# Kernel tuning notes

Hardware: AMD Instinct MI355X
Metric: run time of the kernel (lower is better)

## Reference

```python
import jax, jax.numpy as jnp
import numpy as np

NEG_INF = -1.0e9  # matches the -1000000000.0 additive mask in the source


def setup_inputs() -> dict:
    key = jax.random.key(0)
    kq, kk, kv = jax.random.split(key, 3)
    B, Lq, Lk, D = 16, 2048, 2048, 128
    q = jax.random.normal(kq, (B, Lq, D), dtype=jnp.float32)
    k = jax.random.normal(kk, (B, Lk, D), dtype=jnp.float32)
    v = jax.random.normal(kv, (B, Lk, D), dtype=jnp.float32)
    mask = jnp.ones((B, Lq, Lk), dtype=jnp.int32)  # 1 = attend, 0 = blocked
    return {"q": q, "k": k, "v": v, "mask": mask}


def reference(q, k, v, mask):
    # temper = sqrt(d_k)
    temper = jnp.sqrt(jnp.asarray(q.shape[-1], dtype=jnp.float32))
    # scores: [B, Lq, Lk] = batch_dot(q, k, axes=[2,2]) / temper
    scores = jnp.einsum("bqd,bkd->bqk", q, k) / temper
    # additive mask: -1e9 * (1 - mask)
    scores = scores + NEG_INF * (1.0 - mask.astype(jnp.float32))
    attn = jax.nn.softmax(scores, axis=-1)
    # dropout is identity at inference time
    out = jnp.einsum("bqk,bkd->bqd", attn, v)
    return (out, attn)
```

## Files before the change

kernel.cpp:

```cpp
#include <hip/hip_runtime.h>

typedef __bf16 bf16_t;
typedef __bf16 bf16x8 __attribute__((ext_vector_type(8)));
typedef __bf16 bf16x4 __attribute__((ext_vector_type(4)));
typedef float  f32x4  __attribute__((ext_vector_type(4)));
typedef int    i32x4  __attribute__((ext_vector_type(4)));

#define B_      16
#define L_      2048
#define D_      128
#define QTB     128
#define NEGINF  (-1.0e9f)
#define SCALE   0.08838834764831845f

#define MFMA_BF16 __builtin_amdgcn_mfma_f32_16x16x32_bf16

#define BARRIER() do { asm volatile("s_waitcnt lgkmcnt(0)" ::: "memory"); \
                       __builtin_amdgcn_s_barrier(); } while (0)

__global__ __launch_bounds__(256) void prep_kernel(
    const float* __restrict__ k, const float* __restrict__ v,
    bf16_t* __restrict__ kb, bf16_t* __restrict__ vt)
{
    __shared__ bf16_t tile[128 * 144];
    const int tid = threadIdx.x;
    const int bid = (int)blockIdx.x;

    if (bid < 256) {
        const int b  = bid >> 4;
        const int l0 = (bid & 15) * 128;
        #pragma unroll
        for (int it = 0; it < 16; ++it) {
            int idx = tid + it * 256;
            int row = idx >> 5;
            int dc4 = idx & 31;
            f32x4 x = __builtin_nontemporal_load(
                (const f32x4*)(v + ((size_t)b * L_ + l0 + row) * (size_t)D_ + dc4 * 4));
            #pragma unroll
            for (int i = 0; i < 4; ++i) tile[(dc4 * 4 + i) * 144 + row] = (bf16_t)x[i];
        }
        __syncthreads();
        #pragma unroll
        for (int it = 0; it < 8; ++it) {
            int idx = tid + it * 256;
            int d   = idx >> 4;
            int lc  = idx & 15;
            bf16x8 vec = *(const bf16x8*)&tile[d * 144 + lc * 8];
            *(bf16x8*)(vt + ((size_t)b * D_ + d) * (size_t)L_ + l0 + lc * 8) = vec;
        }
    } else {
        const int idx0 = (bid - 256) * 256 + tid;
        #pragma unroll
        for (int c = 0; c < 16; ++c) {
            int idx = idx0 + c * 65536;
            f32x4 x = __builtin_nontemporal_load((const f32x4*)(k + (size_t)idx * 4));
            bf16x4 o;
            #pragma unroll
            for (int i = 0; i < 4; ++i) o[i] = (bf16_t)x[i];
            *(bf16x4*)(kb + (size_t)idx * 4) = o;
        }
    }
}

template <bool WS>
__global__ __launch_bounds__(512, 1) void sdpa_kernel(
    const float* __restrict__ q, const float* __restrict__ k,
    const float* __restrict__ v, const int* __restrict__ mask,
    const bf16_t* __restrict__ kb, const bf16_t* __restrict__ vt,
    float* __restrict__ out, float* __restrict__ attn)
{
    __shared__ char     Kst[2][16384];
    __shared__ char     MV[2][32768];
    __shared__ unsigned mlds[8 * 1024];
    __shared__ bf16_t   plds[8][16][40];

    const int tid = threadIdx.x;
    const int w   = tid >> 6;
    const int l   = tid & 63;
    const int li  = l & 15;
    const int lg  = l >> 4;

    const int bid  = (int)blockIdx.x;
    const int bid2 = (bid & 7) * 32 + (bid >> 3);
    const int b    = bid2 >> 4;
    const int qt   = bid2 & 15;
    const int qbase = qt * QTB;

    const size_t bq = (size_t)b * L_;

    const float*  qp  = q  + (bq + qbase) * (size_t)D_;
    const bf16_t* kbp = kb + bq * (size_t)D_;
    const float*  kp  = k  + bq * (size_t)D_;
    const bf16_t* vtp = vt + (size_t)b * D_ * (size_t)L_;
    const float*  vp  = v  + bq * (size_t)D_;
    float* attnrow = attn + (bq + qbase + (size_t)(w * 16 + li)) * (size_t)L_;
    float* outp    = out  + (bq + qbase) * (size_t)D_;

    bf16x8 aq[4];
    #pragma unroll
    for (int ds = 0; ds < 4; ++ds) {
        const float* p = qp + (size_t)(w * 16 + li) * D_ + ds * 32 + lg * 8;
        f32x4 x0 = *(const f32x4*)p;
        f32x4 x1 = *(const f32x4*)(p + 4);
        bf16x8 a;
        #pragma unroll
        for (int u = 0; u < 4; ++u) {
            a[u]     = (bf16_t)(x0[u] * SCALE);
            a[4 + u] = (bf16_t)(x1[u] * SCALE);
        }
        aq[ds] = a;
    }

    const int ku_t  = (tid >> 6) & 1;
    const int ku_lg = (tid >> 4) & 3;
    const int ku_li = tid & 15;
    const int ku_ds = tid >> 7;
    const bf16_t* ksrcb = kbp + (size_t)(ku_t * 16 + ku_li) * D_ + ku_ds * 32 + ku_lg * 8;
    const float*  ksrcf = kp  + (size_t)(ku_t * 16 + ku_li) * D_ + ku_ds * 32 + ku_lg * 8;

    const int vu_d  = ((tid >> 6) << 4) | (tid & 15);
    const int vu_lg = (tid >> 4) & 3;
    const bf16_t* vsrcb = vtp + (size_t)vu_d * L_ + vu_lg * 8;

    const int mrow = tid >> 3, mslot = tid & 7;
    const int mdst0 = mrow * 128 + ((mslot * 16) ^ ((mrow & 7) << 4));
    const int mdst1 = (mrow + 64) * 128 + ((mslot * 16) ^ ((mrow & 7) << 4));
    const int*    msrc0 = mask + (size_t)(bq + qbase + mrow) * L_ + mslot * 4;
    const int*    msrc1 = mask + (size_t)(bq + qbase + mrow + 64) * L_ + mslot * 4;

    auto issueK = [&](int t, i32x4 (&ri)[2], f32x4 (&rf)[2][2]) {
        #pragma unroll
        for (int s = 0; s < 2; ++s) {
            if constexpr (WS) {
                ri[s] = *(const i32x4*)(ksrcb + (size_t)(t * 64 + s * 32) * D_);
            } else {
                rf[s][0] = *(const f32x4*)(ksrcf + (size_t)(t * 64 + s * 32) * D_);
                rf[s][1] = *(const f32x4*)(ksrcf + (size_t)(t * 64 + s * 32) * D_ + 4);
            }
        }
    };
    auto writeK = [&](int sl, const i32x4 (&ri)[2], const f32x4 (&rf)[2][2]) {
        #pragma unroll
        for (int s = 0; s < 2; ++s) {
            char* d = Kst[sl] + s * 8192 + tid * 16;
            if constexpr (WS) {
                *(i32x4*)d = ri[s];
            } else {
                bf16x8 o;
                #pragma unroll
                for (int u = 0; u < 4; ++u) { o[u] = (bf16_t)rf[s][0][u]; o[4+u] = (bf16_t)rf[s][1][u]; }
                *(bf16x8*)d = o;
            }
        }
    };
    auto issueM = [&](int t, i32x4 (&m0)[2], i32x4 (&m1)[2]) {
        #pragma unroll
        for (int s = 0; s < 2; ++s) {
            m0[s] = __builtin_nontemporal_load((const i32x4*)(msrc0 + t * 64 + s * 32));
            m1[s] = __builtin_nontemporal_load((const i32x4*)(msrc1 + t * 64 + s * 32));
        }
    };
    auto writeM = [&](int sl, const i32x4 (&m0)[2], const i32x4 (&m1)[2]) {
        #pragma unroll
        for (int s = 0; s < 2; ++s) {
            *(i32x4*)(MV[sl] + s * 16384 + mdst0) = m0[s];
            *(i32x4*)(MV[sl] + s * 16384 + mdst1) = m1[s];
        }
    };
    auto issueV = [&](int t, i32x4 (&ri)[2], float (&vf)[2][8]) {
        #pragma unroll
        for (int s = 0; s < 2; ++s) {
            if constexpr (WS) {
                ri[s] = *(const i32x4*)(vsrcb + t * 64 + s * 32);
            } else {
                #pragma unroll
                for (int u = 0; u < 8; ++u)
                    vf[s][u] = vp[(size_t)(t * 64 + s * 32 + vu_lg * 8 + u) * D_ + vu_d];
            }
        }
    };
    auto writeV = [&](int sl, const i32x4 (&ri)[2], const float (&vf)[2][8]) {
        #pragma unroll
        for (int s = 0; s < 2; ++s) {
            char* d = MV[sl] + s * 8192 + tid * 16;
            if constexpr (WS) {
                *(i32x4*)d = ri[s];
            } else {
                bf16x8 o;
                #pragma unroll
                for (int u = 0; u < 8; ++u) o[u] = (bf16_t)vf[s][u];
                *(bf16x8*)d = o;
            }
        }
    };

    const int xr = (li & 7) << 4;
    const int kbo = lg * 256 + li * 16;

    auto qkt = [&](const char* Ks, f32x4& a0, f32x4& a1) {
        f32x4 r0 = {0.f,0.f,0.f,0.f}, r1 = {0.f,0.f,0.f,0.f};
        #pragma unroll
        for (int ds = 0; ds < 4; ++ds) {
            bf16x8 k0 = *(const bf16x8*)(Ks + ds * 2048 + kbo);
            r0 = MFMA_BF16(k0, aq[ds], r0, 0, 0, 0);
        }
        #pragma unroll
        for (int ds = 0; ds < 4; ++ds) {
            bf16x8 k1 = *(const bf16x8*)(Ks + ds * 2048 + 1024 + kbo);
            r1 = MFMA_BF16(k1, aq[ds], r1, 0, 0, 0);
        }
        a0 = r0; a1 = r1;
    };

    float m_run = -3.4e38f, l_run = 0.f;
    {
        unsigned mword = 0;
        auto p1c = [&](int m, int sl, int s) {
            f32x4 a0, a1;
            qkt(Kst[sl] + s * 8192, a0, a1);
            const char* Ms = MV[sl] + s * 16384 + (w * 16 + li) * 128;
            i32x4 va  = *(const i32x4*)(Ms + ((lg * 16) ^ xr));
            i32x4 vb_ = *(const i32x4*)(Ms + ((64 + lg * 16) ^ xr));
            unsigned byte =
                (va[0]  != 0 ?   1u : 0u) | (va[1]  != 0 ?   2u : 0u) |
                (va[2]  != 0 ?   4u : 0u) | (va[3]  != 0 ?   8u : 0u) |
                (vb_[0] != 0 ?  16u : 0u) | (vb_[1] != 0 ?  32u : 0u) |
                (vb_[2] != 0 ?  64u : 0u) | (vb_[3] != 0 ? 128u : 0u);
            float s0[4], s1[4];
            #pragma unroll
            for (int r = 0; r < 4; ++r) {
                s0[r] = a0[r] + (((byte >> r)       & 1u) ? 0.f : NEGINF);
                s1[r] = a1[r] + (((byte >> (4 + r)) & 1u) ? 0.f : NEGINF);
            }
            float mx = fmaxf(fmaxf(fmaxf(s0[0], s0[1]), fmaxf(s0[2], s0[3])),
                             fmaxf(fmaxf(s1[0], s1[1]), fmaxf(s1[2], s1[3])));
            mx = fmaxf(mx, m_run);
            float acc = 0.f;
            #pragma unroll
            for (int r = 0; r < 4; ++r)
                acc += __expf(s0[r] - mx) + __expf(s1[r] - mx);
            l_run = l_run * __expf(m_run - mx) + acc;
            m_run = mx;
            mword |= byte << ((m & 3) * 8);
            if ((m & 3) == 3) { mlds[w * 1024 + (m >> 2) * 64 + l] = mword; mword = 0; }
        };

        i32x4 kA[2]{}, kB[2]{}, m0A[2]{}, m1A[2]{}, m0B[2]{}, m1B[2]{};
        f32x4 kfA[2][2], kfB[2][2];
        issueK(0, kA, kfA); issueM(0, m0A, m1A);
        issueK(1, kB, kfB); issueM(1, m0B, m1B);
        writeK(0, kA, kfA); writeM(0, m0A, m1A);
        BARRIER();
        #pragma unroll 1
        for (int t = 0; t < 32; t += 2) {
            if (t + 2 < 32) { issueK(t + 2, kA, kfA); issueM(t + 2, m0A, m1A); }
            p1c(2 * t,     0, 0);
            p1c(2 * t + 1, 0, 1);
            writeK(1, kB, kfB); writeM(1, m0B, m1B);
            BARRIER();
            if (t + 3 < 32) { issueK(t + 3, kB, kfB); issueM(t + 3, m0B, m1B); }
            p1c(2 * t + 2, 1, 0);
            p1c(2 * t + 3, 1, 1);
            if (t + 2 < 32) { writeK(0, kA, kfA); writeM(0, m0A, m1A); }
            BARRIER();
        }
    }

    #pragma unroll
    for (int off = 16; off < 64; off <<= 1) {
        float mo = __shfl_xor(m_run, off);
        float lo = __shfl_xor(l_run, off);
        float mn = fmaxf(m_run, mo);
        l_run = l_run * __expf(m_run - mn) + lo * __expf(mo - mn);
        m_run = mn;
    }
    const float inv_l = 1.f / l_run;

    f32x4 pv[8];
    #pragma unroll
    for (int dt = 0; dt < 8; ++dt) pv[dt] = {0.f, 0.f, 0.f, 0.f};

    {
        auto p2c = [&](int m, int sl, int s) {
            f32x4 a0, a1;
            qkt(Kst[sl] + s * 8192, a0, a1);
            const unsigned mw = mlds[w * 1024 + (m >> 2) * 64 + l];
            const unsigned byte = (mw >> ((m & 3) * 8)) & 0xffu;
            f32x4 o0, o1; bf16x4 pb0, pb1;
            #pragma unroll
            for (int r = 0; r < 4; ++r) {
                float sa = a0[r] + (((byte >> r)       & 1u) ? 0.f : NEGINF);
                float sb = a1[r] + (((byte >> (4 + r)) & 1u) ? 0.f : NEGINF);
                float p0 = __expf(sa - m_run);
                float p1 = __expf(sb - m_run);
                o0[r] = p0 * inv_l;  o1[r] = p1 * inv_l;
                pb0[r] = (bf16_t)p0; pb1[r] = (bf16_t)p1;
            }
            __builtin_nontemporal_store(o0, (f32x4*)(attnrow + m * 32 + lg * 4));
            __builtin_nontemporal_store(o1, (f32x4*)(attnrow + m * 32 + 16 + lg * 4));
            *(bf16x4*)&plds[w][li][lg * 4]      = pb0;
            *(bf16x4*)&plds[w][li][16 + lg * 4] = pb1;
            bf16x8 pa = *(const bf16x8*)&plds[w][li][lg * 8];
            const char* Vs = MV[sl] + s * 8192;
            #pragma unroll
            for (int dt = 0; dt < 8; ++dt) {
                bf16x8 vbf = *(const bf16x8*)(Vs + dt * 1024 + kbo);
                pv[dt] = MFMA_BF16(pa, vbf, pv[dt], 0, 0, 0);
            }
        };

        i32x4 kA[2]{}, kB[2]{}, vA[2]{}, vB[2]{};
        f32x4 kfA[2][2], kfB[2][2];
        float vfA[2][8], vfB[2][8];
        issueK(0, kA, kfA); issueV(0, vA, vfA);
        issueK(1, kB, kfB); issueV(1, vB, vfB);
        writeK(0, kA, kfA); writeV(0, vA, vfA);
        BARRIER();
        #pragma unroll 1
        for (int t = 0; t < 32; t += 2) {
            if (t + 2 < 32) { issueK(t + 2, kA, kfA); issueV(t + 2, vA, vfA); }
            p2c(2 * t,     0, 0);
            p2c(2 * t + 1, 0, 1);
            writeK(1, kB, kfB); writeV(1, vB, vfB);
            BARRIER();
            if (t + 3 < 32) { issueK(t + 3, kB, kfB); issueV(t + 3, vB, vfB); }
            p2c(2 * t + 2, 1, 0);
            p2c(2 * t + 3, 1, 1);
            if (t + 2 < 32) { writeK(0, kA, kfA); writeV(0, vA, vfA); }
            BARRIER();
        }
    }

    #pragma unroll
    for (int r = 0; r < 4; ++r) {
        const float il = __shfl(inv_l, lg * 4 + r);
        float* orow = outp + (size_t)(w * 16 + lg * 4 + r) * D_ + li;
        #pragma unroll
        for (int dt = 0; dt < 8; ++dt)
            __builtin_nontemporal_store(pv[dt][r] * il, orow + dt * 16);
    }
}

extern "C" void kernel_launch(void* const* d_in, const int* in_sizes, int n_in,
                              void* d_out, int out_size, void* d_ws, size_t ws_size,
                              hipStream_t stream) {
    const float* q    = (const float*)d_in[0];
    const float* k    = (const float*)d_in[1];
    const float* v    = (const float*)d_in[2];
    const int*   mask = (const int*)d_in[3];

    float* out  = (float*)d_out;
    float* attn = out + (size_t)B_ * L_ * D_;

    const size_t VT_BYTES = (size_t)B_ * D_ * L_ * 2;
    const size_t KB_BYTES = (size_t)B_ * L_ * D_ * 2;
    const bool ws_ok = ws_size >= VT_BYTES + KB_BYTES;
    bf16_t* vt = (bf16_t*)d_ws;
    bf16_t* kb = (bf16_t*)((char*)d_ws + VT_BYTES);

    if (ws_ok) {
        hipLaunchKernelGGL(prep_kernel, dim3(512), dim3(256), 0, stream, k, v, kb, vt);
        hipLaunchKernelGGL(sdpa_kernel<true>, dim3(256), dim3(512), 0, stream,
                           q, k, v, mask, kb, vt, out, attn);
    } else {
        hipLaunchKernelGGL(sdpa_kernel<false>, dim3(256), dim3(512), 0, stream,
                           q, k, v, mask, kb, vt, out, attn);
    }
}
```

Before: 173.6 us.

## Load mask directly into registers and double key tile size in pass one

Pass one no longer stages the int32 mask through LDS. Each lane now loads its own mask row fragment straight from global memory into registers, which removes the mask LDS writes, reads and swizzle. Pass one also processes K in 128-key stages instead of 64, halving the barriers, and the shared memory is reorganised into a 64KB K buffer plus a separate V buffer. The cost is more registers held per thread for the in-flight K and mask data, and less coalesced mask loads, since each lane reads 16 bytes per row.

```diff
diff --git a/kernel.cpp b/kernel.cpp
--- a/kernel.cpp
+++ b/kernel.cpp
@@ -69,8 +69,8 @@
     const bf16_t* __restrict__ kb, const bf16_t* __restrict__ vt,
     float* __restrict__ out, float* __restrict__ attn)
 {
-    __shared__ char     Kst[2][16384];
-    __shared__ char     MV[2][32768];
+    __shared__ char     Kbig[65536];
+    __shared__ char     Vbuf[32768];
     __shared__ unsigned mlds[8 * 1024];
     __shared__ bf16_t   plds[8][16][40];
 
@@ -122,79 +122,8 @@
     const int vu_lg = (tid >> 4) & 3;
     const bf16_t* vsrcb = vtp + (size_t)vu_d * L_ + vu_lg * 8;
 
-    const int mrow = tid >> 3, mslot = tid & 7;
-    const int mdst0 = mrow * 128 + ((mslot * 16) ^ ((mrow & 7) << 4));
-    const int mdst1 = (mrow + 64) * 128 + ((mslot * 16) ^ ((mrow & 7) << 4));
-    const int*    msrc0 = mask + (size_t)(bq + qbase + mrow) * L_ + mslot * 4;
-    const int*    msrc1 = mask + (size_t)(bq + qbase + mrow + 64) * L_ + mslot * 4;
-
-    auto issueK = [&](int t, i32x4 (&ri)[2], f32x4 (&rf)[2][2]) {
-        #pragma unroll
-        for (int s = 0; s < 2; ++s) {
-            if constexpr (WS) {
-                ri[s] = *(const i32x4*)(ksrcb + (size_t)(t * 64 + s * 32) * D_);
-            } else {
-                rf[s][0] = *(const f32x4*)(ksrcf + (size_t)(t * 64 + s * 32) * D_);
-                rf[s][1] = *(const f32x4*)(ksrcf + (size_t)(t * 64 + s * 32) * D_ + 4);
-            }
-        }
-    };
-    auto writeK = [&](int sl, const i32x4 (&ri)[2], const f32x4 (&rf)[2][2]) {
-        #pragma unroll
-        for (int s = 0; s < 2; ++s) {
-            char* d = Kst[sl] + s * 8192 + tid * 16;
-            if constexpr (WS) {
-                *(i32x4*)d = ri[s];
-            } else {
-                bf16x8 o;
-                #pragma unroll
-                for (int u = 0; u < 4; ++u) { o[u] = (bf16_t)rf[s][0][u]; o[4+u] = (bf16_t)rf[s][1][u]; }
-                *(bf16x8*)d = o;
-            }
-        }
-    };
-    auto issueM = [&](int t, i32x4 (&m0)[2], i32x4 (&m1)[2]) {
-        #pragma unroll
-        for (int s = 0; s < 2; ++s) {
-            m0[s] = __builtin_nontemporal_load((const i32x4*)(msrc0 + t * 64 + s * 32));
-            m1[s] = __builtin_nontemporal_load((const i32x4*)(msrc1 + t * 64 + s * 32));
-        }
-    };
-    auto writeM = [&](int sl, const i32x4 (&m0)[2], const i32x4 (&m1)[2]) {
-        #pragma unroll
-        for (int s = 0; s < 2; ++s) {
-            *(i32x4*)(MV[sl] + s * 16384 + mdst0) = m0[s];
-            *(i32x4*)(MV[sl] + s * 16384 + mdst1) = m1[s];
-        }
-    };
-    auto issueV = [&](int t, i32x4 (&ri)[2], float (&vf)[2][8]) {
-        #pragma unroll
-        for (int s = 0; s < 2; ++s) {
-            if constexpr (WS) {
-                ri[s] = *(const i32x4*)(vsrcb + t * 64 + s * 32);
-            } else {
-                #pragma unroll
-                for (int u = 0; u < 8; ++u)
-                    vf[s][u] = vp[(size_t)(t * 64 + s * 32 + vu_lg * 8 + u) * D_ + vu_d];
-            }
-        }
-    };
-    auto writeV = [&](int sl, const i32x4 (&ri)[2], const float (&vf)[2][8]) {
-        #pragma unroll
-        for (int s = 0; s < 2; ++s) {
-            char* d = MV[sl] + s * 8192 + tid * 16;
-            if constexpr (WS) {
-                *(i32x4*)d = ri[s];
-            } else {
-                bf16x8 o;
-                #pragma unroll
-                for (int u = 0; u < 8; ++u) o[u] = (bf16_t)vf[s][u];
-                *(bf16x8*)d = o;
-            }
-        }
-    };
-
-    const int xr = (li & 7) << 4;
+    const int* mrowp = mask + (size_t)(bq + qbase + w * 16 + li) * L_;
+
     const int kbo = lg * 256 + li * 16;
 
     auto qkt = [&](const char* Ks, f32x4& a0, f32x4& a1) {
@@ -214,13 +143,44 @@
 
     float m_run = -3.4e38f, l_run = 0.f;
     {
+        auto issueK4 = [&](int t, i32x4 (&ri)[4], f32x4 (&rf)[4][2]) {
+            #pragma unroll
+            for (int s = 0; s < 4; ++s) {
+                if constexpr (WS) {
+                    ri[s] = *(const i32x4*)(ksrcb + (size_t)(t * 128 + s * 32) * D_);
+                } else {
+                    rf[s][0] = *(const f32x4*)(ksrcf + (size_t)(t * 128 + s * 32) * D_);
+                    rf[s][1] = *(const f32x4*)(ksrcf + (size_t)(t * 128 + s * 32) * D_ + 4);
+                }
+            }
+        };
+        auto writeK4 = [&](int sl, const i32x4 (&ri)[4], const f32x4 (&rf)[4][2]) {
+            #pragma unroll
+            for (int s = 0; s < 4; ++s) {
+                char* d = Kbig + sl * 32768 + s * 8192 + tid * 16;
+                if constexpr (WS) {
+                    *(i32x4*)d = ri[s];
+                } else {
+                    bf16x8 o;
+                    #pragma unroll
+                    for (int u = 0; u < 4; ++u) { o[u] = (bf16_t)rf[s][0][u]; o[4+u] = (bf16_t)rf[s][1][u]; }
+                    *(bf16x8*)d = o;
+                }
+            }
+        };
+        auto issueM4 = [&](int t, i32x4 (&ma)[4], i32x4 (&mb)[4]) {
+            #pragma unroll
+            for (int s = 0; s < 4; ++s) {
+                const int c0 = t * 128 + s * 32;
+                ma[s] = __builtin_nontemporal_load((const i32x4*)(mrowp + c0 + lg * 4));
+                mb[s] = __builtin_nontemporal_load((const i32x4*)(mrowp + c0 + 16 + lg * 4));
+            }
+        };
+
         unsigned mword = 0;
-        auto p1c = [&](int m, int sl, int s) {
+        auto p1c = [&](int m, const char* Ks, i32x4 va, i32x4 vb_) {
             f32x4 a0, a1;
-            qkt(Kst[sl] + s * 8192, a0, a1);
-            const char* Ms = MV[sl] + s * 16384 + (w * 16 + li) * 128;
-            i32x4 va  = *(const i32x4*)(Ms + ((lg * 16) ^ xr));
-            i32x4 vb_ = *(const i32x4*)(Ms + ((64 + lg * 16) ^ xr));
+            qkt(Ks, a0, a1);
             unsigned byte =
                 (va[0]  != 0 ?   1u : 0u) | (va[1]  != 0 ?   2u : 0u) |
                 (va[2]  != 0 ?   4u : 0u) | (va[3]  != 0 ?   8u : 0u) |
@@ -245,23 +205,31 @@
             if ((m & 3) == 3) { mlds[w * 1024 + (m >> 2) * 64 + l] = mword; mword = 0; }
         };
 
-        i32x4 kA[2]{}, kB[2]{}, m0A[2]{}, m1A[2]{}, m0B[2]{}, m1B[2]{};
-        f32x4 kfA[2][2], kfB[2][2];
-        issueK(0, kA, kfA); issueM(0, m0A, m1A);
-        issueK(1, kB, kfB); issueM(1, m0B, m1B);
-        writeK(0, kA, kfA); writeM(0, m0A, m1A);
+        i32x4 kA[4]{}, kB[4]{};
+        f32x4 kfA[4][2], kfB[4][2];
+        i32x4 maA[4]{}, mbA[4]{}, maB[4]{}, mbB[4]{};
+
+        issueK4(0, kA, kfA); issueM4(0, maA, mbA);
+        issueK4(1, kB, kfB); issueM4(1, maB, mbB);
+        writeK4(0, kA, kfA);
         BARRIER();
         #pragma unroll 1
-        for (int t = 0; t < 32; t += 2) {
-            if (t + 2 < 32) { issueK(t + 2, kA, kfA); issueM(t + 2, m0A, m1A); }
-            p1c(2 * t,     0, 0);
-            p1c(2 * t + 1, 0, 1);
-            writeK(1, kB, kfB); writeM(1, m0B, m1B);
+        for (int t = 0; t < 16; t += 2) {
+            if (t + 2 < 16) issueK4(t + 2, kA, kfA);
+            p1c(4 * t + 0, Kbig + 0 * 8192, maA[0], mbA[0]);
+            p1c(4 * t + 1, Kbig + 1 * 8192, maA[1], mbA[1]);
+            p1c(4 * t + 2, Kbig + 2 * 8192, maA[2], mbA[2]);
+            p1c(4 * t + 3, Kbig + 3 * 8192, maA[3], mbA[3]);
+            if (t + 2 < 16) issueM4(t + 2, maA, mbA);
+            writeK4(1, kB, kfB);
             BARRIER();
-            if (t + 3 < 32) { issueK(t + 3, kB, kfB); issueM(t + 3, m0B, m1B); }
-            p1c(2 * t + 2, 1, 0);
-            p1c(2 * t + 3, 1, 1);
-            if (t + 2 < 32) { writeK(0, kA, kfA); writeM(0, m0A, m1A); }
+            if (t + 3 < 16) issueK4(t + 3, kB, kfB);
+            p1c(4 * t + 4, Kbig + 32768 + 0 * 8192, maB[0], mbB[0]);
+            p1c(4 * t + 5, Kbig + 32768 + 1 * 8192, maB[1], mbB[1]);
+            p1c(4 * t + 6, Kbig + 32768 + 2 * 8192, maB[2], mbB[2]);
+            p1c(4 * t + 7, Kbig + 32768 + 3 * 8192, maB[3], mbB[3]);
+            if (t + 3 < 16) issueM4(t + 3, maB, mbB);
+            if (t + 2 < 16) writeK4(0, kA, kfA);
             BARRIER();
         }
     }
@@ -281,9 +249,61 @@
     for (int dt = 0; dt < 8; ++dt) pv[dt] = {0.f, 0.f, 0.f, 0.f};
 
     {
+        auto issueK = [&](int t, i32x4 (&ri)[2], f32x4 (&rf)[2][2]) {
+            #pragma unroll
+            for (int s = 0; s < 2; ++s) {
+                if constexpr (WS) {
+                    ri[s] = *(const i32x4*)(ksrcb + (size_t)(t * 64 + s * 32) * D_);
+                } else {
+                    rf[s][0] = *(const f32x4*)(ksrcf + (size_t)(t * 64 + s * 32) * D_);
+                    rf[s][1] = *(const f32x4*)(ksrcf + (size_t)(t * 64 + s * 32) * D_ + 4);
+                }
+            }
+        };
+        auto writeK = [&](int sl, const i32x4 (&ri)[2], const f32x4 (&rf)[2][2]) {
+            #pragma unroll
+            for (int s = 0; s < 2; ++s) {
+                char* d = Kbig + sl * 16384 + s * 8192 + tid * 16;
+                if constexpr (WS) {
+                    *(i32x4*)d = ri[s];
+                } else {
+                    bf16x8 o;
+                    #pragma unroll
+                    for (int u = 0; u < 4; ++u) { o[u] = (bf16_t)rf[s][0][u]; o[4+u] = (bf16_t)rf[s][1][u]; }
+                    *(bf16x8*)d = o;
+                }
+            }
+        };
+        auto issueV = [&](int t, i32x4 (&ri)[2], float (&vf)[2][8]) {
+            #pragma unroll
+            for (int s = 0; s < 2; ++s) {
+                if constexpr (WS) {
+                    ri[s] = *(const i32x4*)(vsrcb + t * 64 + s * 32);
+                } else {
+                    #pragma unroll
+                    for (int u = 0; u < 8; ++u)
+                        vf[s][u] = vp[(size_t)(t * 64 + s * 32 + vu_lg * 8 + u) * D_ + vu_d];
+                }
+            }
+        };
+        auto writeV = [&](int sl, const i32x4 (&ri)[2], const float (&vf)[2][8]) {
+            #pragma unroll
+            for (int s = 0; s < 2; ++s) {
+                char* d = Vbuf + sl * 16384 + s * 8192 + tid * 16;
+                if constexpr (WS) {
+                    *(i32x4*)d = ri[s];
+                } else {
+                    bf16x8 o;
+                    #pragma unroll
+                    for (int u = 0; u < 8; ++u) o[u] = (bf16_t)vf[s][u];
+                    *(bf16x8*)d = o;
+                }
+            }
+        };
+
         auto p2c = [&](int m, int sl, int s) {
             f32x4 a0, a1;
-            qkt(Kst[sl] + s * 8192, a0, a1);
+            qkt(Kbig + sl * 16384 + s * 8192, a0, a1);
             const unsigned mw = mlds[w * 1024 + (m >> 2) * 64 + l];
             const unsigned byte = (mw >> ((m & 3) * 8)) & 0xffu;
             f32x4 o0, o1; bf16x4 pb0, pb1;
@@ -301,7 +321,7 @@
             *(bf16x4*)&plds[w][li][lg * 4]      = pb0;
             *(bf16x4*)&plds[w][li][16 + lg * 4] = pb1;
             bf16x8 pa = *(const bf16x8*)&plds[w][li][lg * 8];
-            const char* Vs = MV[sl] + s * 8192;
+            const char* Vs = Vbuf + sl * 16384 + s * 8192;
             #pragma unroll
             for (int dt = 0; dt < 8; ++dt) {
                 bf16x8 vbf = *(const bf16x8*)(Vs + dt * 1024 + kbo);
```

Measured after the change: 184.2 us. 6.1% more time.
